# Kernel optimization log

Measured on AMD Instinct MI355X. Metric: run time of the kernel, lower is better.

## Reference

```python
import jax, jax.numpy as jnp
import numpy as np

VOCAB, D_MODEL, HEADS, PAD_ID = 32000, 512, 8, 0
D_K = D_MODEL // HEADS
EPS = 1e-5


def pos_encoding(T, d):
    pos = jnp.arange(T, dtype=jnp.float32)[:, None]              # [T,1]
    freqs = 1.0 / (10000.0 ** (jnp.arange(0, d, 2, dtype=jnp.float32) / d))
    ang = pos * freqs                                            # [T,d/2]
    pe = jnp.zeros((T, d), dtype=jnp.float32)
    pe = pe.at[:, 0::2].set(jnp.sin(ang)).at[:, 1::2].set(jnp.cos(ang))
    return pe


def layer_norm(x, g, b):
    mu = jnp.mean(x, axis=-1, keepdims=True)
    var = jnp.var(x, axis=-1, keepdims=True)
    return (x - mu) * jax.lax.rsqrt(var + EPS) * g + b


def setup_inputs() -> dict:
    key = jax.random.key(0)
    ks = jax.random.split(key, 12)
    B, T = 4, 2048
    s = 0.02
    inp = {
        "tokens": jax.random.randint(ks[0], (B, T), 0, VOCAB),
        "emb": jax.random.normal(ks[1], (VOCAB, D_MODEL), jnp.float32) * s,
        "wq": jax.random.normal(ks[2], (D_MODEL, D_MODEL), jnp.float32) * s,
        "bq": jnp.zeros((D_MODEL,), jnp.float32),
        "wk": jax.random.normal(ks[3], (D_MODEL, D_MODEL), jnp.float32) * s,
        "bk": jnp.zeros((D_MODEL,), jnp.float32),
        "wv": jax.random.normal(ks[4], (D_MODEL, D_MODEL), jnp.float32) * s,
        "bv": jnp.zeros((D_MODEL,), jnp.float32),
        "wo": jax.random.normal(ks[5], (D_MODEL, D_MODEL), jnp.float32) * s,
        "bo": jnp.zeros((D_MODEL,), jnp.float32),
        "w1": jax.random.normal(ks[6], (D_MODEL, 2 * D_MODEL), jnp.float32) * s,
        "b1": jnp.zeros((2 * D_MODEL,), jnp.float32),
        "w2": jax.random.normal(ks[7], (2 * D_MODEL, D_MODEL), jnp.float32) * s,
        "b2": jnp.zeros((D_MODEL,), jnp.float32),
        "ln1_g": jnp.ones((D_MODEL,), jnp.float32),
        "ln1_b": jnp.zeros((D_MODEL,), jnp.float32),
        "ln2_g": jnp.ones((D_MODEL,), jnp.float32),
        "ln2_b": jnp.zeros((D_MODEL,), jnp.float32),
    }
    return inp


def reference(tokens, emb, wq, bq, wk, bk, wv, bv, wo, bo,
              w1, b1, w2, b2, ln1_g, ln1_b, ln2_g, ln2_b):
    B, T = tokens.shape
    x = emb[tokens] * jnp.sqrt(jnp.float32(D_MODEL))             # [B,T,D]
    x = x + pos_encoding(T, D_MODEL)[None]                       # add PE
    q = (x @ wq + bq).reshape(B, T, HEADS, D_K)
    k = (x @ wk + bk).reshape(B, T, HEADS, D_K)
    v = (x @ wv + bv).reshape(B, T, HEADS, D_K)
    scores = jnp.einsum("bqhd,bkhd->bhqk", q, k) / jnp.sqrt(jnp.float32(D_K))
    key_pad_mask = tokens == PAD_ID                              # [B,T]
    neg = jnp.finfo(scores.dtype).min
    scores = jnp.where(key_pad_mask[:, None, None, :], neg, scores)
    attn = jax.nn.softmax(scores, axis=-1)                       # [B,H,T,T]
    av = jnp.einsum("bhqk,bkhd->bqhd", attn, v).reshape(B, T, D_MODEL)
    av = av @ wo + bo
    h = layer_norm(av + x, ln1_g, ln1_b)
    ff = jax.nn.relu(h @ w1 + b1) @ w2 + b2
    out = layer_norm(h + ff, ln2_g, ln2_b)
    return out, key_pad_mask
```

## Files before the change

kernel.cpp:

```cpp
#include <hip/hip_runtime.h>
#include <hip/hip_bf16.h>
#include <math.h>

#define D_MODEL 512
#define HEADS   8
#define D_K     64
#define T_SEQ   2048
#define B_SZ    4
#define NROWS   (B_SZ * T_SEQ)
#define KVB     64
#define KSPLIT  2
#define KHALF   (T_SEQ / KSPLIT)

#define BM 128
#define BN 128
#define BKG 64

typedef __attribute__((ext_vector_type(8))) short short8;
typedef __attribute__((ext_vector_type(4))) float f32x4;
typedef __attribute__((ext_vector_type(4))) ushort bf16x4;
typedef __attribute__((ext_vector_type(4))) unsigned int u32x4;

typedef __attribute__((address_space(1))) const unsigned int as1_uint;
typedef __attribute__((address_space(3))) unsigned int as3_uint;

__device__ __forceinline__ ushort f2bf(float f) {
    union { float f; unsigned u; } v; v.f = f;
    unsigned u = v.u;
    unsigned r = (u + 0x7FFFu + ((u >> 16) & 1u)) >> 16;
    return (ushort)r;
}
__device__ __forceinline__ float bf2f(ushort u) {
    union { unsigned u; float f; } v; v.u = ((unsigned)u) << 16;
    return v.f;
}
__device__ __forceinline__ unsigned pk_bf16(float lo, float hi) {
    unsigned r;
    asm("v_cvt_pk_bf16_f32 %0, %1, %2" : "=v"(r) : "v"(lo), "v"(hi));
    return r;
}

__global__ __launch_bounds__(256) void k_prep(
    const int* __restrict__ tokens, const float* __restrict__ emb,
    const float* __restrict__ wq, const float* __restrict__ wk,
    const float* __restrict__ wv, const float* __restrict__ wo,
    const float* __restrict__ w1, const float* __restrict__ w2,
    const float* __restrict__ bq, const float* __restrict__ bk,
    const float* __restrict__ bv,
    ushort* __restrict__ xb, float* __restrict__ mask_out,
    ushort* __restrict__ wqkvT, ushort* __restrict__ woT,
    ushort* __restrict__ w1T, ushort* __restrict__ w2T,
    float* __restrict__ bqkv, float qsc)
{
    __shared__ ushort tls[32][33];
    int bid = blockIdx.x, tid = threadIdx.x;
    if (bid < 4096) {
        int row = bid * 2 + (tid >> 7);
        int t   = row & (T_SEQ - 1);
        int tok = tokens[row];
        int t2  = tid & 127;
        if (t2 == 0) mask_out[row] = (tok == 0) ? 1.0f : 0.0f;
        const float* e = emb + (size_t)tok * D_MODEL;
#pragma unroll
        for (int i = 0; i < 4; ++i) {
            int d = t2 + 128 * i;
            float freq = exp2f(-(float)(d & ~1) * 0.025952563240330564f);
            float sn, cs;
            sincosf((float)t * freq, &sn, &cs);
            float x = e[d] * 22.627416997969522f + ((d & 1) ? cs : sn);
            xb[(size_t)row * D_MODEL + d] = f2bf(x);
        }
        return;
    }
    const float* src; ushort* dst; float scale = 1.0f; int K, N, bx, by;
    if (bid < 5120) {
        int b = bid - 4096; int z = b >> 8; int rem = b & 255;
        bx = rem & 15; by = rem >> 4; K = 512; N = 512;
        src = (z == 0) ? wq : (z == 1) ? wk : (z == 2) ? wv : wo;
        dst = (z < 3) ? wqkvT + (size_t)z * 512 * 512 : woT;
        scale = (z == 0) ? qsc : 1.0f;
    } else if (bid < 5632) {
        int b = bid - 5120; bx = b & 31; by = b >> 5; K = 512; N = 1024; src = w1; dst = w1T;
    } else if (bid < 6144) {
        int b = bid - 5632; bx = b & 15; by = b >> 4; K = 1024; N = 512; src = w2; dst = w2T;
    } else {
        int i = (bid - 6144) * 256 + tid;
        if (i < 512)       bqkv[i] = bq[i] * qsc;
        else if (i < 1024) bqkv[i] = bk[i - 512];
        else if (i < 1536) bqkv[i] = bv[i - 1024];
        return;
    }
    int tx = tid & 31, ty = tid >> 5;
    int n0 = bx * 32, k0 = by * 32;
#pragma unroll
    for (int i = 0; i < 4; ++i)
        tls[ty + i * 8][tx] = f2bf(src[(size_t)(k0 + ty + i * 8) * N + n0 + tx] * scale);
    __syncthreads();
#pragma unroll
    for (int i = 0; i < 4; ++i)
        dst[(size_t)(n0 + ty + i * 8) * K + k0 + tx] = tls[tx][ty + i * 8];
}

template<int MODE, bool RELU>
__global__ __launch_bounds__(256) void k_gemm_lds(
    const ushort* __restrict__ A, const ushort* __restrict__ BT,
    const float* __restrict__ bias, void* __restrict__ C0,
    void* __restrict__ C1, void* __restrict__ C2,
    int M, int N, int K)
{
    __shared__ __attribute__((aligned(16))) ushort As[2][BM * BKG];
    __shared__ __attribute__((aligned(16))) ushort Bs[2][BN * BKG];

    const int tid = threadIdx.x;
    const int w = tid >> 6, l = tid & 63;
    const int lr = l & 15, lg = l >> 4;
    const int wr = w >> 1, wc = w & 1;

    int bx = blockIdx.x, by = blockIdx.y;
    {
        int nx = gridDim.x, ny = gridDim.y;
        if ((ny & 7) == 0) {
            int lin = bx + nx * by;
            int xcd = lin & 7, idx = lin >> 3;
            int per = ny >> 3;
            by = xcd * per + (idx % per);
            bx = idx / per;
        }
    }
    const int brow0 = by * BM;
    const int bcol0 = bx * BN;
    const int gi0 = w * 256 + l;
    const int swz = lr & 7;

    f32x4 acc[4][4] = {};
    const int nks = K >> 6;

#define STAGE(buf, k0)                                                          \
    {                                                                           \
        _Pragma("unroll")                                                       \
        for (int i = 0; i < 4; ++i) {                                           \
            int gi = gi0 + i * 64;                                              \
            int row = gi >> 3, slot = gi & 7;                                   \
            int g = slot ^ (row & 7);                                           \
            __builtin_amdgcn_global_load_lds(                                   \
                (as1_uint*)(A + (size_t)(brow0 + row) * K + (k0) + g * 8),      \
                (as3_uint*)(&As[buf][gi * 8]), 16, 0, 0);                       \
            __builtin_amdgcn_global_load_lds(                                   \
                (as1_uint*)(BT + (size_t)(bcol0 + row) * K + (k0) + g * 8),     \
                (as3_uint*)(&Bs[buf][gi * 8]), 16, 0, 0);                       \
        }                                                                       \
    }

    STAGE(0, 0);
    __syncthreads();

    int buf = 0;
    for (int ks = 0; ks < nks; ++ks) {
        if (ks + 1 < nks) STAGE(buf ^ 1, (ks + 1) * BKG);
#pragma unroll
        for (int kk = 0; kk < 2; ++kk) {
            short8 af[4], bfr[4];
#pragma unroll
            for (int m = 0; m < 4; ++m) {
                int row = wr * 64 + m * 16 + lr;
                int slot = (kk * 4 + lg) ^ swz;
                af[m] = *(const short8*)(&As[buf][row * 64 + slot * 8]);
            }
#pragma unroll
            for (int n = 0; n < 4; ++n) {
                int row = wc * 64 + n * 16 + lr;
                int slot = (kk * 4 + lg) ^ swz;
                bfr[n] = *(const short8*)(&Bs[buf][row * 64 + slot * 8]);
            }
#pragma unroll
            for (int m = 0; m < 4; ++m)
#pragma unroll
                for (int n = 0; n < 4; ++n)
                    acc[m][n] = __builtin_amdgcn_mfma_f32_16x16x32_bf16(af[m], bfr[n], acc[m][n], 0, 0, 0);
        }
        __syncthreads();
        buf ^= 1;
    }
#undef STAGE

#pragma unroll
    for (int n = 0; n < 4; ++n) {
        int col = bcol0 + wc * 64 + n * 16 + lr;
        float bv = bias[col];
#pragma unroll
        for (int m = 0; m < 4; ++m) {
            int row0 = brow0 + wr * 64 + m * 16 + 4 * lg;
            if constexpr (MODE == 2) {
                int seg = col >> 9, lc = col & 511;
                if (seg == 2) {
                    bf16x4 pk;
#pragma unroll
                    for (int j = 0; j < 4; ++j) pk[j] = f2bf(acc[m][n][j] + bv);
                    *(bf16x4*)((ushort*)C2 + (size_t)lc * M + row0) = pk;
                } else {
                    ushort* dst = (seg == 0) ? (ushort*)C0 : (ushort*)C1;
#pragma unroll
                    for (int j = 0; j < 4; ++j)
                        dst[(size_t)(row0 + j) * 512 + lc] = f2bf(acc[m][n][j] + bv);
                }
            } else if constexpr (MODE == 0) {
#pragma unroll
                for (int j = 0; j < 4; ++j) {
                    float v = acc[m][n][j] + bv;
                    if (RELU) v = fmaxf(v, 0.0f);
                    ((ushort*)C0)[(size_t)(row0 + j) * N + col] = f2bf(v);
                }
            } else {
#pragma unroll
                for (int j = 0; j < 4; ++j)
                    ((float*)C0)[(size_t)(row0 + j) * N + col] = acc[m][n][j] + bv;
            }
        }
    }
}

__global__ __launch_bounds__(512, 8) void k_attn(
    const ushort* __restrict__ Q, const ushort* __restrict__ Kb,
    const ushort* __restrict__ Vt, const int* __restrict__ tokens,
    ushort* __restrict__ O0, ushort* __restrict__ O1,
    float* __restrict__ lp)
{
    __shared__ __attribute__((aligned(16))) ushort Kl[2][KVB * 64];
    __shared__ __attribute__((aligned(16))) ushort Vl[2][KVB * 64];
    __shared__ __attribute__((aligned(16))) ushort Mbh[KHALF];
    __shared__ int padf[KHALF / KVB];

    const int tid = threadIdx.x;
    const int w = tid >> 6, l = tid & 63;
    const int lr = l & 15, lg = l >> 4;
    const int swz = lr & 7;

    int lin = blockIdx.x + 16 * blockIdx.y + 256 * blockIdx.z;
    int xcd = lin & 7, idx = lin >> 3;
    int group = xcd + 8 * (idx >> 4);
    int qt = idx & 15;
    int ks = group & 1;
    int h  = (group >> 1) & 7;
    int b  = group >> 4;

    const int q0  = qt * 128 + w * 16;
    const int kb0 = ks * KHALF;

    const int gi   = w * 64 + l;
    const int srow = gi >> 3;
    const int sg   = gi & 7;
    const int sgx  = sg ^ (srow & 7);
    const ushort* Ksrc = Kb + ((size_t)(b * T_SEQ + kb0) + srow) * D_MODEL + h * D_K + sgx * 8;
    const int kbase = 32 * (sg >> 2) + 8 * ((sg >> 1) & 1) + 4 * (sg & 1);
    const ushort* Vsrc = Vt + (size_t)(h * D_K + srow) * NROWS + b * T_SEQ + kb0 + kbase;
    const int vds = srow * 128 + sgx * 16;

#define KSTAGE(bufi, kt_)                                                       \
    __builtin_amdgcn_global_load_lds(                                           \
        (as1_uint*)(Ksrc + (size_t)(kt_) * KVB * D_MODEL),                      \
        (as3_uint*)(&Kl[bufi][gi * 8]), 16, 0, 0);

    const ushort* Qh = Q + (size_t)b * T_SEQ * D_MODEL + h * D_K;
    short8 aq[2];
#pragma unroll
    for (int c2 = 0; c2 < 2; ++c2)
        aq[c2] = *(const short8*)(Qh + (size_t)(q0 + lr) * D_MODEL + c2 * 32 + 8 * lg);

    const int* tk = tokens + b * T_SEQ + kb0;
#pragma unroll
    for (int it = 0; it < KHALF / 512; ++it) {
        int i = tid + it * 512;
        bool pad = (tk[i] == 0);
        Mbh[i] = pad ? (ushort)0xFF7F : (ushort)0;
        unsigned long long bal = __ballot(pad);
        if (l == 0) padf[it * 8 + w] = (bal != 0ull);
    }

    float l_run = 0.0f;
    f32x4 acc[4] = {};

    {
        bf16x4 va = *(const bf16x4*)(Vsrc);
        bf16x4 vb2 = *(const bf16x4*)(Vsrc + 16);
        KSTAGE(0, 0);
        u32x4 pk = { ((const unsigned*)&va)[0], ((const unsigned*)&va)[1],
                     ((const unsigned*)&vb2)[0], ((const unsigned*)&vb2)[1] };
        *(u32x4*)((char*)Vl[0] + vds) = pk;
    }
    __syncthreads();

    int buf = 0;
    const int NT = KHALF / KVB;
    for (int kt = 0; kt < NT; ++kt) {
        bf16x4 vna, vnb;
        bool more = (kt + 1 < NT);
        if (more) {
            KSTAGE(buf ^ 1, kt + 1);
            vna = *(const bf16x4*)(Vsrc + (kt + 1) * KVB);
            vnb = *(const bf16x4*)(Vsrc + (kt + 1) * KVB + 16);
        }

        const ushort* Kt = Kl[buf];
        const ushort* Vb = Vl[buf];

        f32x4 s[4];
        __builtin_amdgcn_s_setprio(1);
#pragma unroll
        for (int kb = 0; kb < 4; ++kb) {
            f32x4 sf = {};
#pragma unroll
            for (int c2 = 0; c2 < 2; ++c2) {
                short8 bk = *(const short8*)((const char*)Kt
                            + (kb * 16 + lr) * 128 + (((c2 * 4 + lg) ^ swz) * 16));
                sf = __builtin_amdgcn_mfma_f32_16x16x32_bf16(bk, aq[c2], sf, 0, 0, 0);
            }
            s[kb] = sf;
        }
        __builtin_amdgcn_s_setprio(0);

        if (padf[kt]) {
            const ushort* mrow = Mbh + kt * KVB + 4 * lg;
#pragma unroll
            for (int kb = 0; kb < 4; ++kb) {
                bf16x4 m4 = *(const bf16x4*)(mrow + kb * 16);
#pragma unroll
                for (int j = 0; j < 4; ++j) s[kb][j] += bf2f(m4[j]);
            }
        }

        float pv[4][4];
        float ts = 0.0f;
#pragma unroll
        for (int kb = 0; kb < 4; ++kb)
#pragma unroll
            for (int j = 0; j < 4; ++j) {
                float pe = exp2f(s[kb][j]);
                pv[kb][j] = pe;
                ts += pe;
            }
        ts += __shfl_xor(ts, 16);
        ts += __shfl_xor(ts, 32);
        l_run += ts;

        unsigned dw[4][2];
#pragma unroll
        for (int kb = 0; kb < 4; ++kb) {
            dw[kb][0] = pk_bf16(pv[kb][0], pv[kb][1]);
            dw[kb][1] = pk_bf16(pv[kb][2], pv[kb][3]);
        }
        u32x4 pw0 = { dw[0][0], dw[0][1], dw[1][0], dw[1][1] };
        u32x4 pw1 = { dw[2][0], dw[2][1], dw[3][0], dw[3][1] };
        short8 pa0 = __builtin_bit_cast(short8, pw0);
        short8 pa1 = __builtin_bit_cast(short8, pw1);

        __builtin_amdgcn_s_setprio(1);
#pragma unroll
        for (int c = 0; c < 4; ++c) {
            short8 bv0 = *(const short8*)((const char*)Vb
                         + (c * 16 + lr) * 128 + ((lg ^ swz) * 16));
            acc[c] = __builtin_amdgcn_mfma_f32_16x16x32_bf16(bv0, pa0, acc[c], 0, 0, 0);
            short8 bv1 = *(const short8*)((const char*)Vb
                         + (c * 16 + lr) * 128 + (((4 + lg) ^ swz) * 16));
            acc[c] = __builtin_amdgcn_mfma_f32_16x16x32_bf16(bv1, pa1, acc[c], 0, 0, 0);
        }
        __builtin_amdgcn_s_setprio(0);

        if (more) {
            u32x4 pk = { ((const unsigned*)&vna)[0], ((const unsigned*)&vna)[1],
                         ((const unsigned*)&vnb)[0], ((const unsigned*)&vnb)[1] };
            *(u32x4*)((char*)Vl[buf ^ 1] + vds) = pk;
        }
        __syncthreads();
        buf ^= 1;
    }
#undef KSTAGE

    ushort* Op = (ks == 0) ? O0 : O1;
    ushort* orow = Op + (size_t)(b * T_SEQ + q0 + lr) * D_MODEL + h * D_K;
#pragma unroll
    for (int c = 0; c < 4; ++c) {
        bf16x4 pk;
#pragma unroll
        for (int j = 0; j < 4; ++j) pk[j] = f2bf(acc[c][j]);
        *(bf16x4*)(orow + c * 16 + 4 * lg) = pk;
    }
    if (l < 16)
        lp[(size_t)(ks * 8 + h) * NROWS + b * T_SEQ + q0 + l] = l_run;
}

__global__ __launch_bounds__(256) void k_comb(
    ushort* __restrict__ O0, const ushort* __restrict__ O1,
    const float* __restrict__ lp)
{
    int g = blockIdx.x * 256 + threadIdx.x;
    int row = g >> 6, seg = g & 63;
    int h = seg >> 3;
    size_t off = (size_t)row * D_MODEL + seg * 8;
    short8 a = *(const short8*)(O0 + off);
    short8 c = *(const short8*)(O1 + off);
    float l0 = lp[(size_t)h * NROWS + row];
    float l1 = lp[(size_t)(8 + h) * NROWS + row];
    float rl = 1.0f / (l0 + l1);
    short8 r;
#pragma unroll
    for (int i = 0; i < 8; ++i)
        r[i] = (short)f2bf((bf2f((ushort)a[i]) + bf2f((ushort)c[i])) * rl);
    *(short8*)(O0 + off) = r;
}

template<bool A_BF16, bool RES_BF16, bool OUT_F32>
__global__ __launch_bounds__(256) void k_ln(
    const void* __restrict__ A, const void* __restrict__ Res,
    const float* __restrict__ g, const float* __restrict__ bb,
    float* __restrict__ of, ushort* __restrict__ ob)
{
    int row = blockIdx.x * 4 + (threadIdx.x >> 6);
    int l = threadIdx.x & 63;
    float v[8];
    float s = 0.0f, ss = 0.0f;
#pragma unroll
    for (int i = 0; i < 2; ++i) {
        int d0 = i * 256 + l * 4;
        f32x4 va, vb;
        if (A_BF16) {
            bf16x4 t = *(const bf16x4*)((const ushort*)A + (size_t)row * D_MODEL + d0);
#pragma unroll
            for (int j = 0; j < 4; ++j) va[j] = bf2f(t[j]);
        } else {
            va = *(const f32x4*)((const float*)A + (size_t)row * D_MODEL + d0);
        }
        if (RES_BF16) {
            bf16x4 t = *(const bf16x4*)((const ushort*)Res + (size_t)row * D_MODEL + d0);
#pragma unroll
            for (int j = 0; j < 4; ++j) vb[j] = bf2f(t[j]);
        } else {
            vb = *(const f32x4*)((const float*)Res + (size_t)row * D_MODEL + d0);
        }
#pragma unroll
        for (int j = 0; j < 4; ++j) {
            float x = va[j] + vb[j];
            v[i * 4 + j] = x; s += x; ss += x * x;
        }
    }
#pragma unroll
    for (int d = 1; d < 64; d <<= 1) { s += __shfl_xor(s, d); ss += __shfl_xor(ss, d); }
    float mu  = s * (1.0f / 512.0f);
    float var = ss * (1.0f / 512.0f) - mu * mu;
    float rs  = rsqrtf(var + 1e-5f);
#pragma unroll
    for (int i = 0; i < 2; ++i)
#pragma unroll
        for (int j = 0; j < 4; ++j) {
            int d = i * 256 + l * 4 + j;
            float o = (v[i * 4 + j] - mu) * rs * g[d] + bb[d];
            if (OUT_F32) of[(size_t)row * D_MODEL + d] = o;
            else         ob[(size_t)row * D_MODEL + d] = f2bf(o);
        }
}

extern "C" void kernel_launch(void* const* d_in, const int* in_sizes, int n_in,
                              void* d_out, int out_size, void* d_ws, size_t ws_size,
                              hipStream_t stream)
{
    const int*   tokens = (const int*)  d_in[0];
    const float* emb    = (const float*)d_in[1];
    const float* wq     = (const float*)d_in[2];
    const float* bq     = (const float*)d_in[3];
    const float* wk     = (const float*)d_in[4];
    const float* bk     = (const float*)d_in[5];
    const float* wv     = (const float*)d_in[6];
    const float* bv     = (const float*)d_in[7];
    const float* wo     = (const float*)d_in[8];
    const float* bo     = (const float*)d_in[9];
    const float* w1     = (const float*)d_in[10];
    const float* b1     = (const float*)d_in[11];
    const float* w2     = (const float*)d_in[12];
    const float* b2     = (const float*)d_in[13];
    const float* ln1_g  = (const float*)d_in[14];
    const float* ln1_b  = (const float*)d_in[15];
    const float* ln2_g  = (const float*)d_in[16];
    const float* ln2_b  = (const float*)d_in[17];

    char* ws = (char*)d_ws;
    ushort* xb   = (ushort*)(ws + 0);
    ushort* Qb   = (ushort*)(ws + 8388608);
    ushort* Kbuf = (ushort*)(ws + 16777216);
    ushort* Vt   = (ushort*)(ws + 25165824);
    ushort* atb  = (ushort*)(ws + 33554432);
    ushort* AVb  = (ushort*)(ws + 41943040);
    ushort* wqkvT = (ushort*)(ws + 50331648);
    ushort* woT  = wqkvT + 1536 * 512;
    ushort* w1T  = woT + 262144;
    ushort* w2T  = w1T + 524288;
    float*  bqkv = (float*)(w2T + 524288);
    float*  lpart = bqkv + 2048;

    ushort* hb   = Qb;
    ushort* ff1b = Kbuf;
    ushort* ff2b = AVb;

    float* out_f    = (float*)d_out;
    float* mask_out = out_f + (size_t)NROWS * D_MODEL;

    const float QSC = 0.18033688011112042f;

    k_prep<<<6150, 256, 0, stream>>>(
        tokens, emb, wq, wk, wv, wo, w1, w2, bq, bk, bv,
        xb, mask_out, wqkvT, woT, w1T, w2T, bqkv, QSC);

    k_gemm_lds<2, false><<<dim3(12, 64), 256, 0, stream>>>(
        xb, wqkvT, bqkv, Qb, Kbuf, Vt, NROWS, 1536, 512);

    k_attn<<<dim3(16, 16, 4), 512, 0, stream>>>(
        Qb, Kbuf, Vt, tokens, atb, AVb, lpart);
    k_comb<<<2048, 256, 0, stream>>>(atb, AVb, lpart);

    k_gemm_lds<0, false><<<dim3(4, 64), 256, 0, stream>>>(
        atb, woT, bo, AVb, nullptr, nullptr, NROWS, 512, 512);

    k_ln<true, true, false><<<NROWS / 4, 256, 0, stream>>>(
        AVb, xb, ln1_g, ln1_b, nullptr, hb);

    k_gemm_lds<0, true><<<dim3(8, 64), 256, 0, stream>>>(
        hb, w1T, b1, ff1b, nullptr, nullptr, NROWS, 1024, 512);
    k_gemm_lds<0, false><<<dim3(4, 64), 256, 0, stream>>>(
        ff1b, w2T, b2, ff2b, nullptr, nullptr, NROWS, 512, 1024);

    k_ln<true, true, true><<<NROWS / 4, 256, 0, stream>>>(
        ff2b, hb, ln2_g, ln2_b, out_f, nullptr);
}
```

Baseline: 165.8 us.

## Process two query sub-tiles per wave in attention to reuse K/V fragments

Each wave now handles 32 query rows (two 16-row sub-tiles) instead of 16, so every K and V fragment read from LDS feeds twice as many MFMAs. The block covers 256 queries and the grid is halved. The row-sum shuffle reduction moves out of the loop to the epilogue, and the launch bounds drop to 4 blocks per CU to allow more registers. The cost is higher register pressure, lower occupancy, and fewer blocks to spread across the CUs.

Result: no change. 166.1 us (+0.2%).

```diff
diff --git a/kernel.cpp b/kernel.cpp
--- a/kernel.cpp
+++ b/kernel.cpp
@@ -219,7 +219,7 @@
     }
 }
 
-__global__ __launch_bounds__(512, 8) void k_attn(
+__global__ __launch_bounds__(512, 4) void k_attn(
     const ushort* __restrict__ Q, const ushort* __restrict__ Kb,
     const ushort* __restrict__ Vt, const int* __restrict__ tokens,
     ushort* __restrict__ O0, ushort* __restrict__ O1,
@@ -235,15 +235,15 @@
     const int lr = l & 15, lg = l >> 4;
     const int swz = lr & 7;
 
-    int lin = blockIdx.x + 16 * blockIdx.y + 256 * blockIdx.z;
+    int lin = blockIdx.x + 8 * (blockIdx.y + 8 * blockIdx.z);
     int xcd = lin & 7, idx = lin >> 3;
-    int group = xcd + 8 * (idx >> 4);
-    int qt = idx & 15;
-    int ks = group & 1;
-    int h  = (group >> 1) & 7;
-    int b  = group >> 4;
-
-    const int q0  = qt * 128 + w * 16;
+    int qt  = idx & 7;
+    int grp = xcd + 8 * (idx >> 3);
+    int ks  = grp & 1;
+    int h   = (grp >> 1) & 7;
+    int b   = grp >> 4;
+
+    const int q0  = qt * 256 + w * 32;
     const int kb0 = ks * KHALF;
 
     const int gi   = w * 64 + l;
@@ -261,10 +261,13 @@
         (as3_uint*)(&Kl[bufi][gi * 8]), 16, 0, 0);
 
     const ushort* Qh = Q + (size_t)b * T_SEQ * D_MODEL + h * D_K;
-    short8 aq[2];
-#pragma unroll
-    for (int c2 = 0; c2 < 2; ++c2)
-        aq[c2] = *(const short8*)(Qh + (size_t)(q0 + lr) * D_MODEL + c2 * 32 + 8 * lg);
+    short8 aq[2][2];
+#pragma unroll
+    for (int qs = 0; qs < 2; ++qs)
+#pragma unroll
+        for (int c2 = 0; c2 < 2; ++c2)
+            aq[qs][c2] = *(const short8*)(Qh + (size_t)(q0 + qs * 16 + lr) * D_MODEL
+                                          + c2 * 32 + 8 * lg);
 
     const int* tk = tokens + b * T_SEQ + kb0;
 #pragma unroll
@@ -276,8 +279,8 @@
         if (l == 0) padf[it * 8 + w] = (bal != 0ull);
     }
 
-    float l_run = 0.0f;
-    f32x4 acc[4] = {};
+    float l_run[2] = {0.0f, 0.0f};
+    f32x4 acc[2][4] = {};
 
     {
         bf16x4 va = *(const bf16x4*)(Vsrc);
@@ -302,68 +305,70 @@
 
         const ushort* Kt = Kl[buf];
         const ushort* Vb = Vl[buf];
-
-        f32x4 s[4];
-        __builtin_amdgcn_s_setprio(1);
-#pragma unroll
-        for (int kb = 0; kb < 4; ++kb) {
-            f32x4 sf = {};
-#pragma unroll
-            for (int c2 = 0; c2 < 2; ++c2) {
-                short8 bk = *(const short8*)((const char*)Kt
-                            + (kb * 16 + lr) * 128 + (((c2 * 4 + lg) ^ swz) * 16));
-                sf = __builtin_amdgcn_mfma_f32_16x16x32_bf16(bk, aq[c2], sf, 0, 0, 0);
+        bool havePad = padf[kt];
+
+        unsigned dw[2][4][2];
+#pragma unroll
+        for (int kh = 0; kh < 2; ++kh) {
+            short8 kf[2][2];
+#pragma unroll
+            for (int i = 0; i < 2; ++i)
+#pragma unroll
+                for (int c2 = 0; c2 < 2; ++c2)
+                    kf[i][c2] = *(const short8*)((const char*)Kt
+                                + ((2 * kh + i) * 16 + lr) * 128
+                                + (((c2 * 4 + lg) ^ swz) * 16));
+#pragma unroll
+            for (int qs = 0; qs < 2; ++qs)
+#pragma unroll
+                for (int i = 0; i < 2; ++i) {
+                    int kb = 2 * kh + i;
+                    __builtin_amdgcn_s_setprio(1);
+                    f32x4 sf = {};
+                    sf = __builtin_amdgcn_mfma_f32_16x16x32_bf16(kf[i][0], aq[qs][0], sf, 0, 0, 0);
+                    sf = __builtin_amdgcn_mfma_f32_16x16x32_bf16(kf[i][1], aq[qs][1], sf, 0, 0, 0);
+                    __builtin_amdgcn_s_setprio(0);
+                    if (havePad) {
+                        bf16x4 m4 = *(const bf16x4*)(Mbh + kt * KVB + kb * 16 + 4 * lg);
+#pragma unroll
+                        for (int j = 0; j < 4; ++j) sf[j] += bf2f(m4[j]);
+                    }
+                    float p0 = exp2f(sf[0]);
+                    float p1 = exp2f(sf[1]);
+                    float p2 = exp2f(sf[2]);
+                    float p3 = exp2f(sf[3]);
+                    l_run[qs] += (p0 + p1) + (p2 + p3);
+                    dw[qs][kb][0] = pk_bf16(p0, p1);
+                    dw[qs][kb][1] = pk_bf16(p2, p3);
+                }
+        }
+
+#pragma unroll
+        for (int ch = 0; ch < 2; ++ch) {
+            short8 vf[2][2];
+#pragma unroll
+            for (int i = 0; i < 2; ++i)
+#pragma unroll
+                for (int kk = 0; kk < 2; ++kk)
+                    vf[i][kk] = *(const short8*)((const char*)Vb
+                                + ((2 * ch + i) * 16 + lr) * 128
+                                + (((kk * 4 + lg) ^ swz) * 16));
+            __builtin_amdgcn_s_setprio(1);
+#pragma unroll
+            for (int qs = 0; qs < 2; ++qs) {
+                u32x4 pw0 = { dw[qs][0][0], dw[qs][0][1], dw[qs][1][0], dw[qs][1][1] };
+                u32x4 pw1 = { dw[qs][2][0], dw[qs][2][1], dw[qs][3][0], dw[qs][3][1] };
+                short8 pa0 = __builtin_bit_cast(short8, pw0);
+                short8 pa1 = __builtin_bit_cast(short8, pw1);
+#pragma unroll
+                for (int i = 0; i < 2; ++i) {
+                    int c = 2 * ch + i;
+                    acc[qs][c] = __builtin_amdgcn_mfma_f32_16x16x32_bf16(vf[i][0], pa0, acc[qs][c], 0, 0, 0);
+                    acc[qs][c] = __builtin_amdgcn_mfma_f32_16x16x32_bf16(vf[i][1], pa1, acc[qs][c], 0, 0, 0);
+                }
             }
-            s[kb] = sf;
-        }
-        __builtin_amdgcn_s_setprio(0);
-
-        if (padf[kt]) {
-            const ushort* mrow = Mbh + kt * KVB + 4 * lg;
-#pragma unroll
-            for (int kb = 0; kb < 4; ++kb) {
-                bf16x4 m4 = *(const bf16x4*)(mrow + kb * 16);
-#pragma unroll
-                for (int j = 0; j < 4; ++j) s[kb][j] += bf2f(m4[j]);
-            }
-        }
-
-        float pv[4][4];
-        float ts = 0.0f;
-#pragma unroll
-        for (int kb = 0; kb < 4; ++kb)
-#pragma unroll
-            for (int j = 0; j < 4; ++j) {
-                float pe = exp2f(s[kb][j]);
-                pv[kb][j] = pe;
-                ts += pe;
-            }
-        ts += __shfl_xor(ts, 16);
-        ts += __shfl_xor(ts, 32);
-        l_run += ts;
-
-        unsigned dw[4][2];
-#pragma unroll
-        for (int kb = 0; kb < 4; ++kb) {
-            dw[kb][0] = pk_bf16(pv[kb][0], pv[kb][1]);
-            dw[kb][1] = pk_bf16(pv[kb][2], pv[kb][3]);
-        }
-        u32x4 pw0 = { dw[0][0], dw[0][1], dw[1][0], dw[1][1] };
-        u32x4 pw1 = { dw[2][0], dw[2][1], dw[3][0], dw[3][1] };
-        short8 pa0 = __builtin_bit_cast(short8, pw0);
-        short8 pa1 = __builtin_bit_cast(short8, pw1);
-
-        __builtin_amdgcn_s_setprio(1);
-#pragma unroll
-        for (int c = 0; c < 4; ++c) {
-            short8 bv0 = *(const short8*)((const char*)Vb
-                         + (c * 16 + lr) * 128 + ((lg ^ swz) * 16));
-            acc[c] = __builtin_amdgcn_mfma_f32_16x16x32_bf16(bv0, pa0, acc[c], 0, 0, 0);
-            short8 bv1 = *(const short8*)((const char*)Vb
-                         + (c * 16 + lr) * 128 + (((4 + lg) ^ swz) * 16));
-            acc[c] = __builtin_amdgcn_mfma_f32_16x16x32_bf16(bv1, pa1, acc[c], 0, 0, 0);
-        }
-        __builtin_amdgcn_s_setprio(0);
+            __builtin_amdgcn_s_setprio(0);
+        }
 
         if (more) {
             u32x4 pk = { ((const unsigned*)&vna)[0], ((const unsigned*)&vna)[1],
@@ -376,16 +381,22 @@
 #undef KSTAGE
 
     ushort* Op = (ks == 0) ? O0 : O1;
-    ushort* orow = Op + (size_t)(b * T_SEQ + q0 + lr) * D_MODEL + h * D_K;
-#pragma unroll
-    for (int c = 0; c < 4; ++c) {
-        bf16x4 pk;
-#pragma unroll
-        for (int j = 0; j < 4; ++j) pk[j] = f2bf(acc[c][j]);
-        *(bf16x4*)(orow + c * 16 + 4 * lg) = pk;
-    }
-    if (l < 16)
-        lp[(size_t)(ks * 8 + h) * NROWS + b * T_SEQ + q0 + l] = l_run;
+#pragma unroll
+    for (int qs = 0; qs < 2; ++qs) {
+        ushort* orow = Op + (size_t)(b * T_SEQ + q0 + qs * 16 + lr) * D_MODEL + h * D_K;
+#pragma unroll
+        for (int c = 0; c < 4; ++c) {
+            bf16x4 pk;
+#pragma unroll
+            for (int j = 0; j < 4; ++j) pk[j] = f2bf(acc[qs][c][j]);
+            *(bf16x4*)(orow + c * 16 + 4 * lg) = pk;
+        }
+        float ls = l_run[qs];
+        ls += __shfl_xor(ls, 16);
+        ls += __shfl_xor(ls, 32);
+        if (l < 16)
+            lp[(size_t)(ks * 8 + h) * NROWS + b * T_SEQ + q0 + qs * 16 + l] = ls;
+    }
 }
 
 __global__ __launch_bounds__(256) void k_comb(
@@ -511,7 +522,7 @@
     k_gemm_lds<2, false><<<dim3(12, 64), 256, 0, stream>>>(
         xb, wqkvT, bqkv, Qb, Kbuf, Vt, NROWS, 1536, 512);
 
-    k_attn<<<dim3(16, 16, 4), 512, 0, stream>>>(
+    k_attn<<<dim3(8, 8, 8), 512, 0, stream>>>(
         Qb, Kbuf, Vt, tokens, atb, AVb, lpart);
     k_comb<<<2048, 256, 0, stream>>>(atb, AVb, lpart);
 
```
